# Optimization experiments

Measured on AMD Instinct MI355X. Metric: run time of the kernel, lower is better.

Reference implementation:

```python
import jax, jax.numpy as jnp
import numpy as np

DIM = 1024
N_HEADS = 16
HEAD_DIM = DIM // N_HEADS
SCALE = HEAD_DIM ** -0.5


def setup_inputs() -> dict:
    key = jax.random.key(0)
    k_x, k_wqkv, k_bqkv, k_wp, k_bp = jax.random.split(key, 5)
    x = jax.random.normal(k_x, (4, 2048, DIM), dtype=jnp.float32)
    # torch Linear weights: [out_features, in_features]
    w_qkv = jax.random.normal(k_wqkv, (3 * DIM, DIM), dtype=jnp.float32) * (DIM ** -0.5)
    b_qkv = jax.random.normal(k_bqkv, (3 * DIM,), dtype=jnp.float32) * 0.01
    w_proj = jax.random.normal(k_wp, (DIM, DIM), dtype=jnp.float32) * (DIM ** -0.5)
    b_proj = jax.random.normal(k_bp, (DIM,), dtype=jnp.float32) * 0.01
    return {"x": x, "w_qkv": w_qkv, "b_qkv": b_qkv, "w_proj": w_proj, "b_proj": b_proj}


def reference(x, w_qkv, b_qkv, w_proj, b_proj):
    B, N, C = x.shape
    # qkv projection: [B,N,3C] -> [3,B,H,N,hd]
    qkv = x @ w_qkv.T + b_qkv
    qkv = qkv.reshape(B, N, 3, N_HEADS, HEAD_DIM).transpose(2, 0, 3, 1, 4)
    q, k, v = qkv[0], qkv[1], qkv[2]  # each [B,H,N,hd]
    attn = jnp.einsum("bhqd,bhkd->bhqk", q, k) * SCALE  # [B,H,N,N]
    attn = jax.nn.softmax(attn, axis=-1)
    out = jnp.einsum("bhqk,bhkd->bhqd", attn, v)  # [B,H,N,hd]
    out = out.transpose(0, 2, 1, 3).reshape(B, N, C)
    return out @ w_proj.T + b_proj
```

## Files before the change

### kernel.cpp

```cpp
#include <hip/hip_runtime.h>
#include <hip/hip_bf16.h>
#include <stdint.h>


#define DIMC   1024
#define NHEADS 16
#define HDIM   64
#define BATCH  4
#define SEQ    2048
#define MTOT   (BATCH*SEQ)
#define QPRE   0.18033688011112042f

typedef __attribute__((ext_vector_type(8))) short bf16x8;
typedef __attribute__((ext_vector_type(4))) float f32x4;
typedef __attribute__((ext_vector_type(16))) float f32x16;
typedef __attribute__((ext_vector_type(2))) unsigned int u32x2;

static __device__ __forceinline__ short f2bf(float f) {
  union { float f; uint32_t u; } c; c.f = f;
  uint32_t u = c.u;
  return (short)((u + 0x7fffu + ((u >> 16) & 1u)) >> 16);
}
static __device__ __forceinline__ uint32_t pk2bf_t(float lo, float hi) {
  union { float f; uint32_t u; } a, b; a.f = lo; b.f = hi;
  return (a.u >> 16) | (b.u & 0xFFFF0000u);
}
static __device__ __forceinline__ uint32_t pk2bf(float lo, float hi) {
  union { float f; uint32_t u; } a, b; a.f = lo; b.f = hi;
  return ((a.u + 0x8000u) >> 16) | ((b.u + 0x8000u) & 0xFFFF0000u);
}

static __device__ __forceinline__ void gload_lds16(const void* g, void* l) {
  __builtin_amdgcn_global_load_lds(
      (const __attribute__((address_space(1))) void*)g,
      (__attribute__((address_space(3))) void*)l, 16, 0, 0);
}

__global__ void cvt_f32_bf16(const float* __restrict__ s, short* __restrict__ d, int n4) {
  int i = blockIdx.x * blockDim.x + threadIdx.x;
  if (i < n4) {
    float4 v = reinterpret_cast<const float4*>(s)[i];
    short4 o;
    o.x = f2bf(v.x); o.y = f2bf(v.y); o.z = f2bf(v.z); o.w = f2bf(v.w);
    reinterpret_cast<short4*>(d)[i] = o;
  }
}

template <int MODE>
__launch_bounds__(256, 2)
__global__ void gemm_bt(const short* __restrict__ A, const short* __restrict__ Bm,
                        const float* __restrict__ bias,
                        short* __restrict__ q_out, short* __restrict__ k_out,
                        short* __restrict__ vt_out, float* __restrict__ f_out,
                        int Ncols) {
  const int K = 1024;
  __shared__ short lds_a[128 * 64];
  __shared__ short lds_b[128 * 64];
  const int ntiles = Ncols >> 7;
  const int bid = (blockIdx.x & 7) * ((int)gridDim.x >> 3) + ((int)blockIdx.x >> 3);
  const int tm = bid / ntiles, tn = bid % ntiles;
  const int m0 = tm << 7, n0 = tn << 7;
  const int t = threadIdx.x;
  const int wave = t >> 6, lane = t & 63;
  const int wr = wave >> 1, wc = wave & 1;
  const int lo = lane & 15, hi = lane >> 4;

  f32x4 acc[4][4] = {};

  for (int k0 = 0; k0 < K; k0 += 64) {
    __syncthreads();
#pragma unroll
    for (int c = 0; c < 4; ++c) {
      int idx = c * 256 + t;
      int row = idx >> 3, cb = idx & 7;
      gload_lds16(A + (size_t)(m0 + row) * K + k0 + cb * 8,
                  (char*)lds_a + c * 4096 + wave * 1024);
      gload_lds16(Bm + (size_t)(n0 + row) * K + k0 + cb * 8,
                  (char*)lds_b + c * 4096 + wave * 1024);
    }
    __syncthreads();
#pragma unroll
    for (int kk = 0; kk < 2; ++kk) {
      bf16x8 af[4], bfr[4];
#pragma unroll
      for (int mi = 0; mi < 4; ++mi)
        af[mi] = *reinterpret_cast<const bf16x8*>(
            lds_a + (wr * 64 + mi * 16 + lo) * 64 + kk * 32 + hi * 8);
#pragma unroll
      for (int ni = 0; ni < 4; ++ni)
        bfr[ni] = *reinterpret_cast<const bf16x8*>(
            lds_b + (wc * 64 + ni * 16 + lo) * 64 + kk * 32 + hi * 8);
#pragma unroll
      for (int mi = 0; mi < 4; ++mi)
#pragma unroll
        for (int ni = 0; ni < 4; ++ni)
          acc[mi][ni] = __builtin_amdgcn_mfma_f32_16x16x32_bf16(
              af[mi], bfr[ni], acc[mi][ni], 0, 0, 0);
    }
  }

#pragma unroll
  for (int mi = 0; mi < 4; ++mi) {
#pragma unroll
    for (int ni = 0; ni < 4; ++ni) {
      int col = n0 + wc * 64 + ni * 16 + lo;
      float bv = bias[col];
      int rowb = m0 + wr * 64 + mi * 16 + hi * 4;
      if (MODE == 0) {
        int which = col >> 10;
        int hh = (col & 1023) >> 6;
        int d = col & 63;
        int b = rowb >> 11;
        int nq0 = rowb & 2047;
        if (which == 2) {
          short4 pk4;
          pk4.x = f2bf(acc[mi][ni][0] + bv);
          pk4.y = f2bf(acc[mi][ni][1] + bv);
          pk4.z = f2bf(acc[mi][ni][2] + bv);
          pk4.w = f2bf(acc[mi][ni][3] + bv);
          *reinterpret_cast<short4*>(
              vt_out + ((size_t)(b * NHEADS + hh) * HDIM + d) * SEQ + nq0) = pk4;
        } else {
#pragma unroll
          for (int r = 0; r < 4; ++r) {
            float v = acc[mi][ni][r] + bv;
            size_t o = (((size_t)(b * NHEADS + hh) * SEQ) + nq0 + r) * HDIM + d;
            if (which == 0) q_out[o] = f2bf(v * QPRE);
            else            k_out[o] = f2bf(v);
          }
        }
      } else {
#pragma unroll
        for (int r = 0; r < 4; ++r)
          f_out[(size_t)(rowb + r) * Ncols + col] = acc[mi][ni][r] + bv;
      }
    }
  }
}

__launch_bounds__(256, 4)
__global__ void attn_fwd(const short* __restrict__ qb, const short* __restrict__ kb,
                         const short* __restrict__ vtb, short* __restrict__ ao) {
  __shared__ __align__(16) char smem[32768];

  const int t = threadIdx.x, wave = t >> 6, lane = t & 63;
  const int l31 = lane & 31, hi = lane >> 5;

  const int wg = ((int)blockIdx.x & 7) * 128 + ((int)blockIdx.x >> 3);
  const int bh = wg >> 4, qt = wg & 15;
  const int b4 = bh >> 4, h = bh & 15;
  const int q0w = qt * 128 + wave * 32;
  const short* Kp = kb + (size_t)bh * SEQ * HDIM;
  const short* Vtp = vtb + (size_t)bh * HDIM * SEQ;

  const int srow = t >> 3;
  const int fsr  = (srow & 7) ^ (srow >> 3);
  const int ksrc = ((t & 7) ^ fsr) << 3;
  const int vsl0 = ((t & 7) ^ fsr) << 1;
  const int vd   = (vsl0 >> 3) * 32 + srow;
  const int vkv  = (vsl0 & 7) << 2;

  auto stage = [&](int tile, int b) {
    gload_lds16(Kp + (size_t)(tile * 32 + srow) * HDIM + ksrc,
                smem + b * 4096 + t * 16);
    gload_lds16(Vtp + (size_t)vd * SEQ + tile * 32 + vkv,
                smem + 16384 + b * 4096 + t * 16);
  };

  bf16x8 qf[4];
  {
    const short* Qr = qb + (size_t)bh * SEQ * HDIM + (size_t)(q0w + l31) * HDIM + hi * 8;
#pragma unroll
    for (int mk = 0; mk < 4; ++mk)
      qf[mk] = *reinterpret_cast<const bf16x8*>(Qr + mk * 16);
  }
  stage(0, 0);
  stage(1, 1);

  f32x16 acc0, acc1, z16;
#pragma unroll
  for (int r = 0; r < 16; ++r) { acc0[r] = 0.f; acc1[r] = 0.f; z16[r] = 0.f; }
  float l_run = 0.f;

  const int fl  = (l31 & 7) ^ (l31 >> 3);
  const int sw2 = fl << 1;
  union PU { uint32_t u[4]; bf16x8 v; };
  PU ones;
  ones.u[0] = 0x3F803F80u; ones.u[1] = 0x3F803F80u;
  ones.u[2] = 0x3F803F80u; ones.u[3] = 0x3F803F80u;

  asm volatile("s_waitcnt vmcnt(2)" ::: "memory");
  __builtin_amdgcn_s_barrier();
  asm volatile("" ::: "memory");
  f32x16 sPrev;
  {
    const char* Kb = smem;
    bf16x8 kf0 = *reinterpret_cast<const bf16x8*>(Kb + l31 * 128 + ((hi ^ fl) << 4));
    sPrev = __builtin_amdgcn_mfma_f32_32x32x16_bf16(kf0, qf[0], z16, 0, 0, 0);
#pragma unroll
    for (int mk = 1; mk < 4; ++mk) {
      bf16x8 kf = *reinterpret_cast<const bf16x8*>(
          Kb + l31 * 128 + (((mk * 2 + hi) ^ fl) << 4));
      sPrev = __builtin_amdgcn_mfma_f32_32x32x16_bf16(kf, qf[mk], sPrev, 0, 0, 0);
    }
  }

#pragma unroll 4
  for (int i = 1; i < 64; ++i) {
    if (i < 63) {
      stage(i + 1, (i + 1) & 3);
      asm volatile("s_waitcnt vmcnt(2)" ::: "memory");
    } else {
      asm volatile("s_waitcnt vmcnt(0)" ::: "memory");
    }
    __builtin_amdgcn_s_barrier();
    asm volatile("" ::: "memory");

    __builtin_amdgcn_s_setprio(1);
    PU pu0, pu1;
#pragma unroll
    for (int m = 0; m < 4; ++m) {
      pu0.u[m] = pk2bf_t(__builtin_amdgcn_exp2f(sPrev[2 * m]),
                         __builtin_amdgcn_exp2f(sPrev[2 * m + 1]));
      pu1.u[m] = pk2bf_t(__builtin_amdgcn_exp2f(sPrev[8 + 2 * m]),
                         __builtin_amdgcn_exp2f(sPrev[8 + 2 * m + 1]));
    }

    const char* Kb = smem + (i & 3) * 4096;
    bf16x8 kf0 = *reinterpret_cast<const bf16x8*>(Kb + l31 * 128 + ((hi ^ fl) << 4));
    f32x16 sNew = __builtin_amdgcn_mfma_f32_32x32x16_bf16(kf0, qf[0], z16, 0, 0, 0);
#pragma unroll
    for (int mk = 1; mk < 4; ++mk) {
      bf16x8 kf = *reinterpret_cast<const bf16x8*>(
          Kb + l31 * 128 + (((mk * 2 + hi) ^ fl) << 4));
      sNew = __builtin_amdgcn_mfma_f32_32x32x16_bf16(kf, qf[mk], sNew, 0, 0, 0);
    }

    f32x16 ls = __builtin_amdgcn_mfma_f32_32x32x16_bf16(ones.v, pu0.v, z16, 0, 0, 0);
    ls = __builtin_amdgcn_mfma_f32_32x32x16_bf16(ones.v, pu1.v, ls, 0, 0, 0);
    const char* Vb = smem + 16384 + ((i - 1) & 3) * 4096 + l31 * 128;
#pragma unroll
    for (int db = 0; db < 2; ++db) {
#pragma unroll
      for (int mf = 0; mf < 2; ++mf) {
        const int sl = db * 8 + mf * 4 + hi;
        u32x2 alo = *reinterpret_cast<const u32x2*>(Vb + ((sl ^ sw2) << 3));
        u32x2 ahi = *reinterpret_cast<const u32x2*>(Vb + (((sl | 2) ^ sw2) << 3));
        PU vf;
        vf.u[0] = alo[0]; vf.u[1] = alo[1]; vf.u[2] = ahi[0]; vf.u[3] = ahi[1];
        if (db == 0)
          acc0 = __builtin_amdgcn_mfma_f32_32x32x16_bf16(vf.v, (mf ? pu1.v : pu0.v), acc0, 0, 0, 0);
        else
          acc1 = __builtin_amdgcn_mfma_f32_32x32x16_bf16(vf.v, (mf ? pu1.v : pu0.v), acc1, 0, 0, 0);
      }
    }
    __builtin_amdgcn_s_setprio(0);
    l_run += ls[0];

    sPrev = sNew;
  }

  {
    PU pu0, pu1;
#pragma unroll
    for (int m = 0; m < 4; ++m) {
      pu0.u[m] = pk2bf_t(__builtin_amdgcn_exp2f(sPrev[2 * m]),
                         __builtin_amdgcn_exp2f(sPrev[2 * m + 1]));
      pu1.u[m] = pk2bf_t(__builtin_amdgcn_exp2f(sPrev[8 + 2 * m]),
                         __builtin_amdgcn_exp2f(sPrev[8 + 2 * m + 1]));
    }
    f32x16 ls = __builtin_amdgcn_mfma_f32_32x32x16_bf16(ones.v, pu0.v, z16, 0, 0, 0);
    ls = __builtin_amdgcn_mfma_f32_32x32x16_bf16(ones.v, pu1.v, ls, 0, 0, 0);
    const char* Vb = smem + 16384 + 3 * 4096 + l31 * 128;
#pragma unroll
    for (int db = 0; db < 2; ++db) {
#pragma unroll
      for (int mf = 0; mf < 2; ++mf) {
        const int sl = db * 8 + mf * 4 + hi;
        u32x2 alo = *reinterpret_cast<const u32x2*>(Vb + ((sl ^ sw2) << 3));
        u32x2 ahi = *reinterpret_cast<const u32x2*>(Vb + (((sl | 2) ^ sw2) << 3));
        PU vf;
        vf.u[0] = alo[0]; vf.u[1] = alo[1]; vf.u[2] = ahi[0]; vf.u[3] = ahi[1];
        if (db == 0)
          acc0 = __builtin_amdgcn_mfma_f32_32x32x16_bf16(vf.v, (mf ? pu1.v : pu0.v), acc0, 0, 0, 0);
        else
          acc1 = __builtin_amdgcn_mfma_f32_32x32x16_bf16(vf.v, (mf ? pu1.v : pu0.v), acc1, 0, 0, 0);
      }
    }
    l_run += ls[0];
  }

  __syncthreads();
  short* Olp = (short*)smem;
  const float inv = 1.0f / l_run;
#pragma unroll
  for (int db = 0; db < 2; ++db) {
#pragma unroll
    for (int i = 0; i < 8; ++i) {
      int r = 2 * i;
      int d = db * 32 + (r & 3) + 8 * (i >> 1) + 4 * hi;
      float fa = (db ? acc1[r] : acc0[r]) * inv;
      float fb = (db ? acc1[r + 1] : acc0[r + 1]) * inv;
      *reinterpret_cast<uint32_t*>(&Olp[wave * 2304 + l31 * 72 + d]) = pk2bf(fa, fb);
    }
  }
  __syncthreads();
#pragma unroll
  for (int it = 0; it < 4; ++it) {
    int ch = it * 64 + lane;
    int q = ch >> 3, d8 = ch & 7;
    bf16x8 v = *reinterpret_cast<const bf16x8*>(&Olp[wave * 2304 + q * 72 + d8 * 8]);
    *reinterpret_cast<bf16x8*>(
        ao + (((size_t)b4 * SEQ + q0w + q) * NHEADS + h) * HDIM + d8 * 8) = v;
  }
}

extern "C" void kernel_launch(void* const* d_in, const int* in_sizes, int n_in,
                              void* d_out, int out_size, void* d_ws, size_t ws_size,
                              hipStream_t stream) {
  const float* x      = (const float*)d_in[0];
  const float* w_qkv  = (const float*)d_in[1];
  const float* b_qkv  = (const float*)d_in[2];
  const float* w_proj = (const float*)d_in[3];
  const float* b_proj = (const float*)d_in[4];
  float* out = (float*)d_out;

  char* ws = (char*)d_ws;
  short* xb    = (short*)(ws);
  short* wqkvb = (short*)(ws + 16777216);
  short* wpb   = (short*)(ws + 16777216 + 6291456);
  short* qb    = (short*)(ws + 25165824);
  short* kb    = (short*)(ws + 25165824 + 16777216);
  short* vtb   = (short*)(ws + 25165824 + 2 * 16777216);
  short* aob   = (short*)(ws + 25165824 + 3 * 16777216);

  cvt_f32_bf16<<<8192, 256, 0, stream>>>(x, xb, MTOT * DIMC / 4);
  cvt_f32_bf16<<<3072, 256, 0, stream>>>(w_qkv, wqkvb, 3 * DIMC * DIMC / 4);
  cvt_f32_bf16<<<1024, 256, 0, stream>>>(w_proj, wpb, DIMC * DIMC / 4);

  gemm_bt<0><<<(MTOT / 128) * (3 * DIMC / 128), 256, 0, stream>>>(
      xb, wqkvb, b_qkv, qb, kb, vtb, nullptr, 3 * DIMC);

  attn_fwd<<<64 * 16, 256, 0, stream>>>(qb, kb, vtb, aob);

  gemm_bt<1><<<(MTOT / 128) * (DIMC / 128), 256, 0, stream>>>(
      aob, wpb, b_proj, nullptr, nullptr, nullptr, out, DIMC);
}
```

Before: 198.5 us.

## Triple-buffer GEMM K loop with swizzled LDS and compute V^T as separate GEMM

The GEMM main loop moves from a two-barrier, 64-wide K step to a triple-buffered 32-wide K pipeline. Global-to-LDS loads for the next tile are issued before computing the current one, and an XOR swizzle is applied to the LDS layout to avoid bank conflicts. Occupancy hint rises to 3 blocks per CU. The V projection is split into its own GEMM (MODE 2) that computes V^T directly as W_v·x^T, writing coalesced rows of a [H*D, B*N] layout instead of strided short4 transposed stores. Attention V addressing is updated to the new layout. This adds a kernel launch and more LDS per block.

```diff
diff --git a/kernel.cpp b/kernel.cpp
--- a/kernel.cpp
+++ b/kernel.cpp
@@ -47,15 +47,15 @@
 }
 
 template <int MODE>
-__launch_bounds__(256, 2)
+__launch_bounds__(256, 3)
 __global__ void gemm_bt(const short* __restrict__ A, const short* __restrict__ Bm,
                         const float* __restrict__ bias,
                         short* __restrict__ q_out, short* __restrict__ k_out,
                         short* __restrict__ vt_out, float* __restrict__ f_out,
                         int Ncols) {
   const int K = 1024;
-  __shared__ short lds_a[128 * 64];
-  __shared__ short lds_b[128 * 64];
+  __shared__ __align__(16) short lds_a[3 * 4096];
+  __shared__ __align__(16) short lds_b[3 * 4096];
   const int ntiles = Ncols >> 7;
   const int bid = (blockIdx.x & 7) * ((int)gridDim.x >> 3) + ((int)blockIdx.x >> 3);
   const int tm = bid / ntiles, tn = bid % ntiles;
@@ -65,38 +65,56 @@
   const int wr = wave >> 1, wc = wave & 1;
   const int lo = lane & 15, hi = lane >> 4;
 
+  const int r0 = t >> 2, sl0 = t & 3;
+
+  auto stage = [&](int kt, int b) {
+    const int k0 = kt << 5;
+#pragma unroll
+    for (int c = 0; c < 2; ++c) {
+      const int row = c * 64 + r0;
+      const int ssl = sl0 ^ ((row ^ (row >> 2)) & 3);
+      gload_lds16(A + (size_t)(m0 + row) * K + k0 + ssl * 8,
+                  (char*)lds_a + b * 8192 + c * 4096 + t * 16);
+      gload_lds16(Bm + (size_t)(n0 + row) * K + k0 + ssl * 8,
+                  (char*)lds_b + b * 8192 + c * 4096 + t * 16);
+    }
+  };
+
+  stage(0, 0);
+
   f32x4 acc[4][4] = {};
-
-  for (int k0 = 0; k0 < K; k0 += 64) {
-    __syncthreads();
-#pragma unroll
-    for (int c = 0; c < 4; ++c) {
-      int idx = c * 256 + t;
-      int row = idx >> 3, cb = idx & 7;
-      gload_lds16(A + (size_t)(m0 + row) * K + k0 + cb * 8,
-                  (char*)lds_a + c * 4096 + wave * 1024);
-      gload_lds16(Bm + (size_t)(n0 + row) * K + k0 + cb * 8,
-                  (char*)lds_b + c * 4096 + wave * 1024);
-    }
-    __syncthreads();
-#pragma unroll
-    for (int kk = 0; kk < 2; ++kk) {
-      bf16x8 af[4], bfr[4];
-#pragma unroll
-      for (int mi = 0; mi < 4; ++mi)
-        af[mi] = *reinterpret_cast<const bf16x8*>(
-            lds_a + (wr * 64 + mi * 16 + lo) * 64 + kk * 32 + hi * 8);
+  const int flo = (lo ^ (lo >> 2)) & 3;
+  const int roff = ((hi ^ flo) << 3);
+
+  int cur = 0, nxt = 1;
+  for (int i = 0; i < 32; ++i) {
+    if (i < 31) {
+      stage(i + 1, nxt);
+      asm volatile("s_waitcnt vmcnt(4)" ::: "memory");
+    } else {
+      asm volatile("s_waitcnt vmcnt(0)" ::: "memory");
+    }
+    __builtin_amdgcn_s_barrier();
+    asm volatile("" ::: "memory");
+
+    const short* Ab = lds_a + cur * 4096;
+    const short* Bb = lds_b + cur * 4096;
+    bf16x8 af[4], bfr[4];
+#pragma unroll
+    for (int mi = 0; mi < 4; ++mi)
+      af[mi] = *reinterpret_cast<const bf16x8*>(Ab + (wr * 64 + mi * 16 + lo) * 32 + roff);
+#pragma unroll
+    for (int ni = 0; ni < 4; ++ni)
+      bfr[ni] = *reinterpret_cast<const bf16x8*>(Bb + (wc * 64 + ni * 16 + lo) * 32 + roff);
+#pragma unroll
+    for (int mi = 0; mi < 4; ++mi)
 #pragma unroll
       for (int ni = 0; ni < 4; ++ni)
-        bfr[ni] = *reinterpret_cast<const bf16x8*>(
-            lds_b + (wc * 64 + ni * 16 + lo) * 64 + kk * 32 + hi * 8);
-#pragma unroll
-      for (int mi = 0; mi < 4; ++mi)
-#pragma unroll
-        for (int ni = 0; ni < 4; ++ni)
-          acc[mi][ni] = __builtin_amdgcn_mfma_f32_16x16x32_bf16(
-              af[mi], bfr[ni], acc[mi][ni], 0, 0, 0);
-    }
+        acc[mi][ni] = __builtin_amdgcn_mfma_f32_16x16x32_bf16(
+            af[mi], bfr[ni], acc[mi][ni], 0, 0, 0);
+
+    asm volatile("" ::: "memory");
+    cur = nxt; nxt = (nxt == 2) ? 0 : nxt + 1;
   }
 
 #pragma unroll
@@ -104,35 +122,30 @@
 #pragma unroll
     for (int ni = 0; ni < 4; ++ni) {
       int col = n0 + wc * 64 + ni * 16 + lo;
-      float bv = bias[col];
       int rowb = m0 + wr * 64 + mi * 16 + hi * 4;
       if (MODE == 0) {
+        float bv = bias[col];
         int which = col >> 10;
         int hh = (col & 1023) >> 6;
         int d = col & 63;
         int b = rowb >> 11;
         int nq0 = rowb & 2047;
-        if (which == 2) {
-          short4 pk4;
-          pk4.x = f2bf(acc[mi][ni][0] + bv);
-          pk4.y = f2bf(acc[mi][ni][1] + bv);
-          pk4.z = f2bf(acc[mi][ni][2] + bv);
-          pk4.w = f2bf(acc[mi][ni][3] + bv);
-          *reinterpret_cast<short4*>(
-              vt_out + ((size_t)(b * NHEADS + hh) * HDIM + d) * SEQ + nq0) = pk4;
-        } else {
-#pragma unroll
-          for (int r = 0; r < 4; ++r) {
-            float v = acc[mi][ni][r] + bv;
-            size_t o = (((size_t)(b * NHEADS + hh) * SEQ) + nq0 + r) * HDIM + d;
-            if (which == 0) q_out[o] = f2bf(v * QPRE);
-            else            k_out[o] = f2bf(v);
-          }
+#pragma unroll
+        for (int r = 0; r < 4; ++r) {
+          float v = acc[mi][ni][r] + bv;
+          size_t o = (((size_t)(b * NHEADS + hh) * SEQ) + nq0 + r) * HDIM + d;
+          if (which == 0) q_out[o] = f2bf(v * QPRE);
+          else            k_out[o] = f2bf(v);
         }
-      } else {
+      } else if (MODE == 1) {
+        float bv = bias[col];
 #pragma unroll
         for (int r = 0; r < 4; ++r)
           f_out[(size_t)(rowb + r) * Ncols + col] = acc[mi][ni][r] + bv;
+      } else {
+#pragma unroll
+        for (int r = 0; r < 4; ++r)
+          vt_out[(size_t)(rowb + r) * Ncols + col] = f2bf(acc[mi][ni][r] + bias[rowb + r]);
       }
     }
   }
@@ -151,7 +164,7 @@
   const int b4 = bh >> 4, h = bh & 15;
   const int q0w = qt * 128 + wave * 32;
   const short* Kp = kb + (size_t)bh * SEQ * HDIM;
-  const short* Vtp = vtb + (size_t)bh * HDIM * SEQ;
+  const short* Vtp = vtb + (size_t)h * HDIM * MTOT + (size_t)b4 * SEQ;
 
   const int srow = t >> 3;
   const int fsr  = (srow & 7) ^ (srow >> 3);
@@ -163,7 +176,7 @@
   auto stage = [&](int tile, int b) {
     gload_lds16(Kp + (size_t)(tile * 32 + srow) * HDIM + ksrc,
                 smem + b * 4096 + t * 16);
-    gload_lds16(Vtp + (size_t)vd * SEQ + tile * 32 + vkv,
+    gload_lds16(Vtp + (size_t)vd * MTOT + tile * 32 + vkv,
                 smem + 16384 + b * 4096 + t * 16);
   };
 
@@ -338,8 +351,12 @@
   cvt_f32_bf16<<<3072, 256, 0, stream>>>(w_qkv, wqkvb, 3 * DIMC * DIMC / 4);
   cvt_f32_bf16<<<1024, 256, 0, stream>>>(w_proj, wpb, DIMC * DIMC / 4);
 
-  gemm_bt<0><<<(MTOT / 128) * (3 * DIMC / 128), 256, 0, stream>>>(
-      xb, wqkvb, b_qkv, qb, kb, vtb, nullptr, 3 * DIMC);
+  gemm_bt<0><<<(MTOT / 128) * (2 * DIMC / 128), 256, 0, stream>>>(
+      xb, wqkvb, b_qkv, qb, kb, nullptr, nullptr, 2 * DIMC);
+
+  gemm_bt<2><<<(DIMC / 128) * (MTOT / 128), 256, 0, stream>>>(
+      wqkvb + (size_t)2 * DIMC * DIMC, xb, b_qkv + 2 * DIMC,
+      nullptr, nullptr, vtb, nullptr, MTOT);
 
   attn_fwd<<<64 * 16, 256, 0, stream>>>(qb, kb, vtb, aob);
 
```

Measured after the change: 204.6 us. 1.03x slower.

## Stage QKV epilogue through LDS, compute V^T as separate GEMM, fuse conversions

Applied to the files above, without the earlier changes.

Merges the three f32-to-bf16 conversion launches into one kernel. The QKV GEMM epilogue now writes into a padded LDS tile and then issues coalesced 16-byte stores, instead of scattered 2-byte stores. V is computed by a separate transposed GEMM (W_v times x^T) that writes V^T directly in a [head, d, token] layout, and attention indexing is updated to match. Occupancy hint is raised to 3 blocks per CU, at the cost of extra LDS traffic and barriers in the epilogue.

```diff
diff --git a/kernel.cpp b/kernel.cpp
--- a/kernel.cpp
+++ b/kernel.cpp
@@ -36,26 +36,31 @@
       (__attribute__((address_space(3))) void*)l, 16, 0, 0);
 }
 
-__global__ void cvt_f32_bf16(const float* __restrict__ s, short* __restrict__ d, int n4) {
+__global__ void cvt_all(const float* __restrict__ x, const float* __restrict__ wq,
+                        const float* __restrict__ wp, short* __restrict__ xb,
+                        short* __restrict__ wqb, short* __restrict__ wpb) {
   int i = blockIdx.x * blockDim.x + threadIdx.x;
-  if (i < n4) {
-    float4 v = reinterpret_cast<const float4*>(s)[i];
-    short4 o;
-    o.x = f2bf(v.x); o.y = f2bf(v.y); o.z = f2bf(v.z); o.w = f2bf(v.w);
-    reinterpret_cast<short4*>(d)[i] = o;
-  }
+  const float* s; short* d;
+  if (i < 2097152)      { s = x;  d = xb;  }
+  else if (i < 2883584) { s = wq; d = wqb; i -= 2097152; }
+  else                  { s = wp; d = wpb; i -= 2883584; }
+  float4 v = reinterpret_cast<const float4*>(s)[i];
+  short4 o;
+  o.x = f2bf(v.x); o.y = f2bf(v.y); o.z = f2bf(v.z); o.w = f2bf(v.w);
+  reinterpret_cast<short4*>(d)[i] = o;
 }
 
 template <int MODE>
-__launch_bounds__(256, 2)
+__launch_bounds__(256, 3)
 __global__ void gemm_bt(const short* __restrict__ A, const short* __restrict__ Bm,
                         const float* __restrict__ bias,
                         short* __restrict__ q_out, short* __restrict__ k_out,
                         short* __restrict__ vt_out, float* __restrict__ f_out,
                         int Ncols) {
   const int K = 1024;
-  __shared__ short lds_a[128 * 64];
-  __shared__ short lds_b[128 * 64];
+  __shared__ __align__(16) char gsmem[34816];
+  short* lds_a = (short*)gsmem;
+  short* lds_b = (short*)(gsmem + 16384);
   const int ntiles = Ncols >> 7;
   const int bid = (blockIdx.x & 7) * ((int)gridDim.x >> 3) + ((int)blockIdx.x >> 3);
   const int tm = bid / ntiles, tn = bid % ntiles;
@@ -74,9 +79,9 @@
       int idx = c * 256 + t;
       int row = idx >> 3, cb = idx & 7;
       gload_lds16(A + (size_t)(m0 + row) * K + k0 + cb * 8,
-                  (char*)lds_a + c * 4096 + wave * 1024);
+                  gsmem + c * 4096 + wave * 1024);
       gload_lds16(Bm + (size_t)(n0 + row) * K + k0 + cb * 8,
-                  (char*)lds_b + c * 4096 + wave * 1024);
+                  gsmem + 16384 + c * 4096 + wave * 1024);
     }
     __syncthreads();
 #pragma unroll
@@ -99,40 +104,51 @@
     }
   }
 
-#pragma unroll
-  for (int mi = 0; mi < 4; ++mi) {
-#pragma unroll
-    for (int ni = 0; ni < 4; ++ni) {
-      int col = n0 + wc * 64 + ni * 16 + lo;
-      float bv = bias[col];
-      int rowb = m0 + wr * 64 + mi * 16 + hi * 4;
-      if (MODE == 0) {
-        int which = col >> 10;
-        int hh = (col & 1023) >> 6;
-        int d = col & 63;
-        int b = rowb >> 11;
-        int nq0 = rowb & 2047;
-        if (which == 2) {
-          short4 pk4;
-          pk4.x = f2bf(acc[mi][ni][0] + bv);
-          pk4.y = f2bf(acc[mi][ni][1] + bv);
-          pk4.z = f2bf(acc[mi][ni][2] + bv);
-          pk4.w = f2bf(acc[mi][ni][3] + bv);
-          *reinterpret_cast<short4*>(
-              vt_out + ((size_t)(b * NHEADS + hh) * HDIM + d) * SEQ + nq0) = pk4;
-        } else {
-#pragma unroll
-          for (int r = 0; r < 4; ++r) {
-            float v = acc[mi][ni][r] + bv;
-            size_t o = (((size_t)(b * NHEADS + hh) * SEQ) + nq0 + r) * HDIM + d;
-            if (which == 0) q_out[o] = f2bf(v * QPRE);
-            else            k_out[o] = f2bf(v);
-          }
-        }
-      } else {
+  if (MODE == 1) {
+#pragma unroll
+    for (int mi = 0; mi < 4; ++mi)
+#pragma unroll
+      for (int ni = 0; ni < 4; ++ni) {
+        int col = n0 + wc * 64 + ni * 16 + lo;
+        float bv = bias[col];
+        int rowb = m0 + wr * 64 + mi * 16 + hi * 4;
 #pragma unroll
         for (int r = 0; r < 4; ++r)
           f_out[(size_t)(rowb + r) * Ncols + col] = acc[mi][ni][r] + bv;
+      }
+  } else {
+    __syncthreads();
+    short* Cl = (short*)gsmem;
+    const float scale = (MODE == 0 && n0 < 1024) ? QPRE : 1.0f;
+#pragma unroll
+    for (int mi = 0; mi < 4; ++mi)
+#pragma unroll
+      for (int ni = 0; ni < 4; ++ni) {
+        int coll = wc * 64 + ni * 16 + lo;
+        float bvc = (MODE == 0) ? bias[n0 + coll] : 0.f;
+#pragma unroll
+        for (int r = 0; r < 4; ++r) {
+          int rowl = wr * 64 + mi * 16 + hi * 4 + r;
+          float bv = (MODE == 2) ? bias[m0 + rowl] : bvc;
+          Cl[rowl * 136 + coll] = f2bf((acc[mi][ni][r] + bv) * scale);
+        }
+      }
+    __syncthreads();
+#pragma unroll
+    for (int it = 0; it < 8; ++it) {
+      int id = it * 256 + t;
+      int row = id >> 4, c = id & 15;
+      bf16x8 val = *reinterpret_cast<const bf16x8*>(Cl + row * 136 + c * 8);
+      if (MODE == 0) {
+        int token = m0 + row;
+        int colg = n0 + c * 8;
+        int hh = (colg & 1023) >> 6, d = colg & 63;
+        int b = token >> 11, nq = token & 2047;
+        size_t o = (((size_t)(b * NHEADS + hh) * SEQ) + nq) * HDIM + d;
+        if (n0 < 1024) *reinterpret_cast<bf16x8*>(q_out + o) = val;
+        else           *reinterpret_cast<bf16x8*>(k_out + o) = val;
+      } else {
+        *reinterpret_cast<bf16x8*>(vt_out + (size_t)(m0 + row) * Ncols + n0 + c * 8) = val;
       }
     }
   }
@@ -151,7 +167,7 @@
   const int b4 = bh >> 4, h = bh & 15;
   const int q0w = qt * 128 + wave * 32;
   const short* Kp = kb + (size_t)bh * SEQ * HDIM;
-  const short* Vtp = vtb + (size_t)bh * HDIM * SEQ;
+  const short* Vtp = vtb + (size_t)h * HDIM * MTOT + (size_t)b4 * SEQ;
 
   const int srow = t >> 3;
   const int fsr  = (srow & 7) ^ (srow >> 3);
@@ -163,7 +179,7 @@
   auto stage = [&](int tile, int b) {
     gload_lds16(Kp + (size_t)(tile * 32 + srow) * HDIM + ksrc,
                 smem + b * 4096 + t * 16);
-    gload_lds16(Vtp + (size_t)vd * SEQ + tile * 32 + vkv,
+    gload_lds16(Vtp + (size_t)vd * MTOT + tile * 32 + vkv,
                 smem + 16384 + b * 4096 + t * 16);
   };
 
@@ -334,12 +350,14 @@
   short* vtb   = (short*)(ws + 25165824 + 2 * 16777216);
   short* aob   = (short*)(ws + 25165824 + 3 * 16777216);
 
-  cvt_f32_bf16<<<8192, 256, 0, stream>>>(x, xb, MTOT * DIMC / 4);
-  cvt_f32_bf16<<<3072, 256, 0, stream>>>(w_qkv, wqkvb, 3 * DIMC * DIMC / 4);
-  cvt_f32_bf16<<<1024, 256, 0, stream>>>(w_proj, wpb, DIMC * DIMC / 4);
-
-  gemm_bt<0><<<(MTOT / 128) * (3 * DIMC / 128), 256, 0, stream>>>(
-      xb, wqkvb, b_qkv, qb, kb, vtb, nullptr, 3 * DIMC);
+  cvt_all<<<12288, 256, 0, stream>>>(x, w_qkv, w_proj, xb, wqkvb, wpb);
+
+  gemm_bt<0><<<(MTOT / 128) * (2 * DIMC / 128), 256, 0, stream>>>(
+      xb, wqkvb, b_qkv, qb, kb, nullptr, nullptr, 2 * DIMC);
+
+  gemm_bt<2><<<(DIMC / 128) * (MTOT / 128), 256, 0, stream>>>(
+      wqkvb + (size_t)2 * DIMC * DIMC, xb, b_qkv + 2 * DIMC,
+      nullptr, nullptr, vtb, nullptr, MTOT);
 
   attn_fwd<<<64 * 16, 256, 0, stream>>>(qb, kb, vtb, aob);
 
```

Result: slower. 211.7 us (+6.6%).

## Load K fragments directly from global into registers, stage only V in LDS

Applied to the files above, without the earlier changes.

Stops staging K tiles through LDS. Each lane now reads its K MFMA fragments straight from global memory into registers at the top of every iteration, and only V^T keeps going through the async LDS ring, which lets shared memory shrink. The vmcnt waits are retuned to cover the extra four outstanding global loads per iteration. This removes the LDS write/read traffic and swizzle for K and may raise occupancy, but puts global-load latency on the QK^T path with only about one iteration of lookahead. It also makes every wave fetch K separately instead of sharing one staged copy.

```diff
diff --git a/kernel.cpp b/kernel.cpp
--- a/kernel.cpp
+++ b/kernel.cpp
@@ -141,7 +141,7 @@
 __launch_bounds__(256, 4)
 __global__ void attn_fwd(const short* __restrict__ qb, const short* __restrict__ kb,
                          const short* __restrict__ vtb, short* __restrict__ ao) {
-  __shared__ __align__(16) char smem[32768];
+  __shared__ __align__(16) char smem[18432];
 
   const int t = threadIdx.x, wave = t >> 6, lane = t & 63;
   const int l31 = lane & 31, hi = lane >> 5;
@@ -155,16 +155,13 @@
 
   const int srow = t >> 3;
   const int fsr  = (srow & 7) ^ (srow >> 3);
-  const int ksrc = ((t & 7) ^ fsr) << 3;
   const int vsl0 = ((t & 7) ^ fsr) << 1;
   const int vd   = (vsl0 >> 3) * 32 + srow;
   const int vkv  = (vsl0 & 7) << 2;
 
-  auto stage = [&](int tile, int b) {
-    gload_lds16(Kp + (size_t)(tile * 32 + srow) * HDIM + ksrc,
+  auto stageV = [&](int tile, int b) {
+    gload_lds16(Vtp + (size_t)vd * SEQ + tile * 32 + vkv,
                 smem + b * 4096 + t * 16);
-    gload_lds16(Vtp + (size_t)vd * SEQ + tile * 32 + vkv,
-                smem + 16384 + b * 4096 + t * 16);
   };
 
   bf16x8 qf[4];
@@ -174,8 +171,15 @@
     for (int mk = 0; mk < 4; ++mk)
       qf[mk] = *reinterpret_cast<const bf16x8*>(Qr + mk * 16);
   }
-  stage(0, 0);
-  stage(1, 1);
+  bf16x8 kf[4];
+  {
+    const short* Kr = Kp + (size_t)l31 * HDIM + hi * 8;
+#pragma unroll
+    for (int mk = 0; mk < 4; ++mk)
+      kf[mk] = *reinterpret_cast<const bf16x8*>(Kr + mk * 16);
+  }
+  stageV(0, 0);
+  stageV(1, 1);
 
   f32x16 acc0, acc1, z16;
 #pragma unroll
@@ -189,29 +193,24 @@
   ones.u[0] = 0x3F803F80u; ones.u[1] = 0x3F803F80u;
   ones.u[2] = 0x3F803F80u; ones.u[3] = 0x3F803F80u;
 
-  asm volatile("s_waitcnt vmcnt(2)" ::: "memory");
-  __builtin_amdgcn_s_barrier();
-  asm volatile("" ::: "memory");
-  f32x16 sPrev;
-  {
-    const char* Kb = smem;
-    bf16x8 kf0 = *reinterpret_cast<const bf16x8*>(Kb + l31 * 128 + ((hi ^ fl) << 4));
-    sPrev = __builtin_amdgcn_mfma_f32_32x32x16_bf16(kf0, qf[0], z16, 0, 0, 0);
-#pragma unroll
-    for (int mk = 1; mk < 4; ++mk) {
-      bf16x8 kf = *reinterpret_cast<const bf16x8*>(
-          Kb + l31 * 128 + (((mk * 2 + hi) ^ fl) << 4));
-      sPrev = __builtin_amdgcn_mfma_f32_32x32x16_bf16(kf, qf[mk], sPrev, 0, 0, 0);
-    }
-  }
+  f32x16 sPrev = __builtin_amdgcn_mfma_f32_32x32x16_bf16(kf[0], qf[0], z16, 0, 0, 0);
+#pragma unroll
+  for (int mk = 1; mk < 4; ++mk)
+    sPrev = __builtin_amdgcn_mfma_f32_32x32x16_bf16(kf[mk], qf[mk], sPrev, 0, 0, 0);
 
 #pragma unroll 4
   for (int i = 1; i < 64; ++i) {
+    {
+      const short* Kr = Kp + (size_t)(i * 32 + l31) * HDIM + hi * 8;
+#pragma unroll
+      for (int mk = 0; mk < 4; ++mk)
+        kf[mk] = *reinterpret_cast<const bf16x8*>(Kr + mk * 16);
+    }
     if (i < 63) {
-      stage(i + 1, (i + 1) & 3);
-      asm volatile("s_waitcnt vmcnt(2)" ::: "memory");
+      stageV(i + 1, (i + 1) & 3);
+      asm volatile("s_waitcnt vmcnt(5)" ::: "memory");
     } else {
-      asm volatile("s_waitcnt vmcnt(0)" ::: "memory");
+      asm volatile("s_waitcnt vmcnt(4)" ::: "memory");
     }
     __builtin_amdgcn_s_barrier();
     asm volatile("" ::: "memory");
@@ -226,19 +225,14 @@
                          __builtin_amdgcn_exp2f(sPrev[8 + 2 * m + 1]));
     }
 
-    const char* Kb = smem + (i & 3) * 4096;
-    bf16x8 kf0 = *reinterpret_cast<const bf16x8*>(Kb + l31 * 128 + ((hi ^ fl) << 4));
-    f32x16 sNew = __builtin_amdgcn_mfma_f32_32x32x16_bf16(kf0, qf[0], z16, 0, 0, 0);
-#pragma unroll
-    for (int mk = 1; mk < 4; ++mk) {
-      bf16x8 kf = *reinterpret_cast<const bf16x8*>(
-          Kb + l31 * 128 + (((mk * 2 + hi) ^ fl) << 4));
-      sNew = __builtin_amdgcn_mfma_f32_32x32x16_bf16(kf, qf[mk], sNew, 0, 0, 0);
-    }
+    f32x16 sNew = __builtin_amdgcn_mfma_f32_32x32x16_bf16(kf[0], qf[0], z16, 0, 0, 0);
+#pragma unroll
+    for (int mk = 1; mk < 4; ++mk)
+      sNew = __builtin_amdgcn_mfma_f32_32x32x16_bf16(kf[mk], qf[mk], sNew, 0, 0, 0);
 
     f32x16 ls = __builtin_amdgcn_mfma_f32_32x32x16_bf16(ones.v, pu0.v, z16, 0, 0, 0);
     ls = __builtin_amdgcn_mfma_f32_32x32x16_bf16(ones.v, pu1.v, ls, 0, 0, 0);
-    const char* Vb = smem + 16384 + ((i - 1) & 3) * 4096 + l31 * 128;
+    const char* Vb = smem + ((i - 1) & 3) * 4096 + l31 * 128;
 #pragma unroll
     for (int db = 0; db < 2; ++db) {
 #pragma unroll
@@ -271,7 +265,7 @@
     }
     f32x16 ls = __builtin_amdgcn_mfma_f32_32x32x16_bf16(ones.v, pu0.v, z16, 0, 0, 0);
     ls = __builtin_amdgcn_mfma_f32_32x32x16_bf16(ones.v, pu1.v, ls, 0, 0, 0);
-    const char* Vb = smem + 16384 + 3 * 4096 + l31 * 128;
+    const char* Vb = smem + 3 * 4096 + l31 * 128;
 #pragma unroll
     for (int db = 0; db < 2; ++db) {
 #pragma unroll
```

After: 240.2 us. +21.0%, slower.
